# Performance work log

Hardware: AMD Instinct MI355X
Metric: run time of the kernel (lower is better)

The kernel has to match this reference:

```python
import jax, jax.numpy as jnp
import numpy as np
import math

B, L, D = 2, 2048, 512
D_INNER, D_STATE, D_CONV = 2 * D, 16, 4
DT_RANK = math.ceil(D / 16)  # 32


def setup_inputs() -> dict:
    key = jax.random.key(0)
    ks = jax.random.split(key, 9)
    s = 0.02
    x = jax.random.normal(ks[0], (B, L, D), dtype=jnp.float32)
    W_in = jax.random.normal(ks[1], (D, 2 * D_INNER), dtype=jnp.float32) * s
    conv_w = jax.random.normal(ks[2], (D_INNER, D_CONV), dtype=jnp.float32) * s
    conv_b = jnp.zeros((D_INNER,), dtype=jnp.float32)
    W_x = jax.random.normal(ks[3], (D_INNER, DT_RANK + 2 * D_STATE), dtype=jnp.float32) * s
    W_dt = jax.random.normal(ks[4], (DT_RANK, D_INNER), dtype=jnp.float32) * s
    b_dt = jax.random.normal(ks[5], (D_INNER,), dtype=jnp.float32) * s
    # S4D-real init: A = -[1..d_state] per channel
    A_log = jnp.log(jnp.broadcast_to(jnp.arange(1, D_STATE + 1, dtype=jnp.float32), (D_INNER, D_STATE)))
    D_param = jnp.ones((D_INNER,), dtype=jnp.float32)
    W_out = jax.random.normal(ks[6], (D_INNER, D), dtype=jnp.float32) * s
    return {"x": x, "W_in": W_in, "conv_w": conv_w, "conv_b": conv_b,
            "W_x": W_x, "W_dt": W_dt, "b_dt": b_dt, "A_log": A_log,
            "D_param": D_param, "W_out": W_out}


def _mamba(x, W_in, conv_w, conv_b, W_x, W_dt, b_dt, A_log, D_param, W_out):
    # in_proj -> [u, z]
    xz = jnp.einsum('bld,de->ble', x, W_in)
    u, z = jnp.split(xz, 2, axis=-1)  # each (B, L, d_inner)
    # depthwise causal conv1d along L
    u_c = jnp.transpose(u, (0, 2, 1))  # (B, d_inner, L)
    kern = conv_w[:, None, :]          # (d_inner, 1, d_conv)
    u_c = jax.lax.conv_general_dilated(
        u_c, kern, window_strides=(1,), padding=[(D_CONV - 1, 0)],
        feature_group_count=D_INNER,
        dimension_numbers=('NCH', 'OIH', 'NCH')) + conv_b[None, :, None]
    u = jax.nn.silu(jnp.transpose(u_c, (0, 2, 1)))  # (B, L, d_inner)
    # input-dependent dt, B, C
    x_dbl = jnp.einsum('bld,de->ble', u, W_x)
    dt_r = x_dbl[..., :DT_RANK]
    Bm = x_dbl[..., DT_RANK:DT_RANK + D_STATE]          # (B, L, d_state)
    Cm = x_dbl[..., DT_RANK + D_STATE:]                  # (B, L, d_state)
    dt = jax.nn.softplus(jnp.einsum('blr,rd->bld', dt_r, W_dt) + b_dt)  # (B, L, d_inner)
    A = -jnp.exp(A_log)  # (d_inner, d_state)

    def step(h, inp):
        dt_t, B_t, C_t, u_t = inp  # (B,d_inner), (B,d_state), (B,d_state), (B,d_inner)
        dA = jnp.exp(dt_t[:, :, None] * A)                      # (B, d_inner, d_state)
        h = h * dA + (dt_t * u_t)[:, :, None] * B_t[:, None, :]
        y = jnp.einsum('bds,bs->bd', h, C_t)
        return h, y

    h0 = jnp.zeros((B, D_INNER, D_STATE), dtype=x.dtype)
    xs = (jnp.transpose(dt, (1, 0, 2)), jnp.transpose(Bm, (1, 0, 2)),
          jnp.transpose(Cm, (1, 0, 2)), jnp.transpose(u, (1, 0, 2)))
    _, ys = jax.lax.scan(step, h0, xs)
    y = jnp.transpose(ys, (1, 0, 2)) + u * D_param  # (B, L, d_inner)
    y = y * jax.nn.silu(z)
    return jnp.einsum('bld,de->ble', y, W_out)


def reference(x, W_in, conv_w, conv_b, W_x, W_dt, b_dt, A_log, D_param, W_out):
    # MambaLayer.forward (eval): out = x + drop_path(mamba(x)); drop_path == Identity at eval
    return x + _mamba(x, W_in, conv_w, conv_b, W_x, W_dt, b_dt, A_log, D_param, W_out)
```

## Files before the change

kernel.cpp:

```cpp
#include <hip/hip_runtime.h>
#include <math.h>

#define BB 2
#define LL 2048
#define DD 512
#define DIN 1024
#define DXZ 2048
#define DSTATE 16
#define DTRANK 32
#define NDBL 64
#define ML (BB*LL)
#define LC2 64
#define NCH2 (LL/LC2)
#define CP 68

typedef __bf16 bf16_t;
typedef bf16_t bf16x8 __attribute__((ext_vector_type(8)));
typedef bf16_t bf16x4 __attribute__((ext_vector_type(4)));
typedef float f32x4 __attribute__((ext_vector_type(4)));

#define GBK 32
#define GBKP 40

__device__ __forceinline__ float fast_silu(float x) {
  return x * __builtin_amdgcn_rcpf(1.f + __builtin_amdgcn_exp2f(-1.44269504f * x));
}

template <int TM, int TN, int MODE, int CT>
__launch_bounds__(256)
__global__ void gemm_mfma(const bf16_t* __restrict__ A,
                          const bf16_t* __restrict__ Bt,
                          float* __restrict__ C, int ldc,
                          int M, int N, int K,
                          const float* __restrict__ aux) {
  __shared__ __align__(16) bf16_t As[TM * GBKP];
  __shared__ __align__(16) bf16_t Bs[TN * GBKP];
  const int tid = threadIdx.x;
  const int wid = tid >> 6, lane = tid & 63;
  const int q = lane >> 4, ln = lane & 15;
  constexpr int WM = TM / 2, WN = TN / 2;
  constexpr int FM = WM / 16, FN = WN / 16;
  const int wm = (wid >> 1) * WM, wn = (wid & 1) * WN;
  const int mBase = blockIdx.y * TM, nBase = blockIdx.x * TN;

  f32x4 acc[FM][FN] = {};

  for (int k0 = 0; k0 < K; k0 += GBK) {
#pragma unroll
    for (int i = 0; i < TM * GBK / (256 * 8); i++) {
      const int slot = tid + i * 256;
      const int m = slot >> 2, k8 = (slot & 3) * 8;
      *(bf16x8*)&As[m * GBKP + k8] =
          *(const bf16x8*)&A[(size_t)(mBase + m) * K + k0 + k8];
    }
#pragma unroll
    for (int i = 0; i < TN * GBK / (256 * 8); i++) {
      const int slot = tid + i * 256;
      const int n = slot >> 2, k8 = (slot & 3) * 8;
      *(bf16x8*)&Bs[n * GBKP + k8] =
          *(const bf16x8*)&Bt[(size_t)(nBase + n) * K + k0 + k8];
    }
    __syncthreads();
    bf16x8 af[FM], bfr[FN];
#pragma unroll
    for (int i = 0; i < FM; i++)
      af[i] = *(const bf16x8*)&As[(wm + i * 16 + ln) * GBKP + q * 8];
#pragma unroll
    for (int j = 0; j < FN; j++)
      bfr[j] = *(const bf16x8*)&Bs[(wn + j * 16 + ln) * GBKP + q * 8];
#pragma unroll
    for (int i = 0; i < FM; i++)
#pragma unroll
      for (int j = 0; j < FN; j++)
        acc[i][j] = __builtin_amdgcn_mfma_f32_16x16x32_bf16(
            af[i], bfr[j], acc[i][j], 0, 0, 0);
    __syncthreads();
  }

#pragma unroll
  for (int i = 0; i < FM; i++) {
    const int m0 = mBase + wm + i * 16 + q * 4;
#pragma unroll
    for (int j = 0; j < FN; j++) {
      const int n = nBase + wn + j * 16 + ln;
      if (CT == 1) {
        *(f32x4*)&C[(size_t)n * ldc + m0] = acc[i][j];
      } else {
#pragma unroll
        for (int r = 0; r < 4; r++) {
          float v = acc[i][j][r];
          if (MODE == 2) v += aux[(size_t)(m0 + r) * ldc + n];
          C[(size_t)(m0 + r) * ldc + n] = v;
        }
      }
    }
  }
}

__global__ void cast_bf16(const float* __restrict__ in, bf16_t* __restrict__ out,
                          int n4) {
  const int i = blockIdx.x * 256 + threadIdx.x;
  if (i >= n4) return;
  const float4 v = ((const float4*)in)[i];
  bf16x4 o = {(bf16_t)v.x, (bf16_t)v.y, (bf16_t)v.z, (bf16_t)v.w};
  ((bf16x4*)out)[i] = o;
}

__launch_bounds__(256)
__global__ void transpose_cast(const float* __restrict__ in, bf16_t* __restrict__ out,
                               int R, int C) {
  __shared__ float T[64][65];
  const int t = threadIdx.x;
  const int rB = blockIdx.y * 64, cB = blockIdx.x * 64;
  {
    const int r = t >> 4, c4 = (t & 15) * 4;
#pragma unroll
    for (int i = 0; i < 4; i++) {
      const float4 v = *(const float4*)&in[(size_t)(rB + r + i * 16) * C + cB + c4];
      T[r + i * 16][c4] = v.x;
      T[r + i * 16][c4 + 1] = v.y;
      T[r + i * 16][c4 + 2] = v.z;
      T[r + i * 16][c4 + 3] = v.w;
    }
  }
  __syncthreads();
  {
    const int c = t >> 2;
#pragma unroll
    for (int i = 0; i < 4; i++) {
      const int r0 = (t & 3) * 16 + i * 4;
      bf16x4 o = {(bf16_t)T[r0][c], (bf16_t)T[r0 + 1][c],
                  (bf16_t)T[r0 + 2][c], (bf16_t)T[r0 + 3][c]};
      *(bf16x4*)&out[(size_t)(cB + c) * R + rB + r0] = o;
    }
  }
}

template <int MODE, int AT, int CT>
__launch_bounds__(256)
__global__ void gemm_tiled(const float* __restrict__ A, int lda,
                           const float* __restrict__ B, int ldb,
                           float* __restrict__ C, int ldc,
                           int M, int N, int K,
                           const float* __restrict__ aux) {
  __shared__ float As[16][68];
  __shared__ float Bs[16][68];

  const int tid = threadIdx.x;
  const int tx = tid & 15, ty = tid >> 4;
  const int mBase = blockIdx.y * 64;
  const int nBase = blockIdx.x * 64;

  float acc[4][4] = {};

  for (int k0 = 0; k0 < K; k0 += 16) {
#pragma unroll
    for (int i = 0; i < 4; i++) {
      int idx = tid + i * 256;
      if (AT == 0) {
        int m = idx >> 4, kk = idx & 15;
        As[kk][m] = A[(size_t)(mBase + m) * lda + k0 + kk];
      } else {
        int kk = idx >> 6, m = idx & 63;
        As[kk][m] = A[(size_t)(k0 + kk) * lda + mBase + m];
      }
    }
#pragma unroll
    for (int i = 0; i < 4; i++) {
      int idx = tid + i * 256;
      int kk = idx >> 6, n = idx & 63;
      Bs[kk][n] = B[(size_t)(k0 + kk) * ldb + nBase + n];
    }
    __syncthreads();
#pragma unroll
    for (int kk = 0; kk < 16; kk++) {
      const float4 a4 = *reinterpret_cast<const float4*>(&As[kk][ty * 4]);
      const float4 b4 = *reinterpret_cast<const float4*>(&Bs[kk][tx * 4]);
      const float a[4] = {a4.x, a4.y, a4.z, a4.w};
      const float b[4] = {b4.x, b4.y, b4.z, b4.w};
#pragma unroll
      for (int i = 0; i < 4; i++)
#pragma unroll
        for (int j = 0; j < 4; j++) acc[i][j] = fmaf(a[i], b[j], acc[i][j]);
    }
    __syncthreads();
  }

  if (CT == 0) {
#pragma unroll
    for (int i = 0; i < 4; i++) {
      const int m = mBase + ty * 4 + i;
      const int n0 = nBase + tx * 4;
      float v[4];
#pragma unroll
      for (int j = 0; j < 4; j++) {
        float x = acc[i][j];
        if (MODE == 1) {
          x += aux[n0 + j];
          x = (x > 20.f) ? x
              : 0.69314718f * __builtin_amdgcn_logf(
                    1.f + __builtin_amdgcn_exp2f(x * 1.44269504f));
        }
        v[j] = x;
      }
      *reinterpret_cast<float4*>(&C[(size_t)m * ldc + n0]) =
          make_float4(v[0], v[1], v[2], v[3]);
    }
  } else {
    const int m0 = mBase + ty * 4;
#pragma unroll
    for (int j = 0; j < 4; j++) {
      const int n = nBase + tx * 4 + j;
      float v[4];
#pragma unroll
      for (int i = 0; i < 4; i++) {
        float x = acc[i][j];
        if (MODE == 1) {
          x += aux[n];
          x = (x > 20.f) ? x
              : 0.69314718f * __builtin_amdgcn_logf(
                    1.f + __builtin_amdgcn_exp2f(x * 1.44269504f));
        }
        v[i] = x;
      }
      *reinterpret_cast<float4*>(&C[(size_t)n * ldc + m0]) =
          make_float4(v[0], v[1], v[2], v[3]);
    }
  }
}

__launch_bounds__(256)
__global__ void conv_silu_T(const float* __restrict__ xzT,
                            const float* __restrict__ conv_w,
                            const float* __restrict__ conv_b,
                            float* __restrict__ uT) {
  const int idx = blockIdx.x * 256 + threadIdx.x;
  const int d = idx >> 10;
  const int ml0 = (idx & 1023) * 4;
  const int l0 = ml0 & (LL - 1);
  const float* row = xzT + (size_t)d * ML + ml0;
  const float4 Bv = *reinterpret_cast<const float4*>(row);
  float4 Av = make_float4(0.f, 0.f, 0.f, 0.f);
  if (l0 != 0) Av = *reinterpret_cast<const float4*>(row - 4);
  const float w0 = conv_w[d * 4 + 0], w1 = conv_w[d * 4 + 1];
  const float w2 = conv_w[d * 4 + 2], w3 = conv_w[d * 4 + 3];
  const float bias = conv_b[d];
  float o[4];
  o[0] = bias + w0 * Av.y + w1 * Av.z + w2 * Av.w + w3 * Bv.x;
  o[1] = bias + w0 * Av.z + w1 * Av.w + w2 * Bv.x + w3 * Bv.y;
  o[2] = bias + w0 * Av.w + w1 * Bv.x + w2 * Bv.y + w3 * Bv.z;
  o[3] = bias + w0 * Bv.x + w1 * Bv.y + w2 * Bv.z + w3 * Bv.w;
#pragma unroll
  for (int i = 0; i < 4; i++) o[i] = fast_silu(o[i]);
  *reinterpret_cast<float4*>(uT + (size_t)d * ML + ml0) =
      make_float4(o[0], o[1], o[2], o[3]);
}

__launch_bounds__(128, 3)
__global__ void scan_fused3(const float* __restrict__ dtT,
                            const float* __restrict__ uT,
                            float* __restrict__ xzT,
                            const float* __restrict__ xdbl,
                            const float* __restrict__ A_log,
                            const float* __restrict__ D_param) {
  __shared__ float dt_s[NCH2 * CP];
  __shared__ float u_s[NCH2 * CP];
  __shared__ float Pc[NCH2][DSTATE];
  __shared__ float Hc[NCH2][DSTATE];

  const int tid = threadIdx.x;
  const int c = blockIdx.x;
  const int b = c >> 10, d = c & (DIN - 1);
  const size_t rowoff = (size_t)d * ML + (size_t)b * LL;
  const float* dtrow = dtT + rowoff;
  const float* urow  = uT + rowoff;
  const float* zrow  = xzT + (size_t)(DIN + d) * ML + (size_t)b * LL;
  float* yrow = xzT + rowoff;

#pragma unroll
  for (int i = 0; i < 4; i++) {
    const int idx = (tid + i * 128) * 4;
    const int la = (idx >> 6) * CP + (idx & 63);
    *(float4*)&dt_s[la] = *(const float4*)&dtrow[idx];
    *(float4*)&u_s[la]  = *(const float4*)&urow[idx];
  }

  const int ch = tid >> 2, q = tid & 3;
  const int s0 = q * 4;
  float Al2[4];
#pragma unroll
  for (int k = 0; k < 4; k++)
    Al2[k] = -expf(A_log[d * DSTATE + s0 + k]) * 1.44269504f;
  const float* dp = dt_s + ch * CP;
  float* up = u_s + ch * CP;
  const float* BC = xdbl + ((size_t)b * LL + (size_t)ch * LC2) * NDBL + DTRANK + s0;
  __syncthreads();

  {
    float h0 = 0.f, h1 = 0.f, h2 = 0.f, h3 = 0.f, sdt = 0.f;
    float4 Bcur[4];
#pragma unroll
    for (int i = 0; i < 4; i++)
      Bcur[i] = *(const float4*)(BC + (size_t)i * NDBL);
    for (int g = 0; g < 16; g++) {
      float4 Bnxt[4];
#pragma unroll
      for (int i = 0; i < 4; i++)
        Bnxt[i] = *(const float4*)(BC + (size_t)((g + 1) * 4 + i) * NDBL);
#pragma unroll
      for (int i = 0; i < 4; i++) {
        const int l = g * 4 + i;
        const float dtv = dp[l];
        const float dtu = dtv * up[l];
        sdt += dtv;
        const float e0 = __builtin_amdgcn_exp2f(dtv * Al2[0]);
        const float e1 = __builtin_amdgcn_exp2f(dtv * Al2[1]);
        const float e2 = __builtin_amdgcn_exp2f(dtv * Al2[2]);
        const float e3 = __builtin_amdgcn_exp2f(dtv * Al2[3]);
        h0 = fmaf(h0, e0, dtu * Bcur[i].x);
        h1 = fmaf(h1, e1, dtu * Bcur[i].y);
        h2 = fmaf(h2, e2, dtu * Bcur[i].z);
        h3 = fmaf(h3, e3, dtu * Bcur[i].w);
      }
#pragma unroll
      for (int i = 0; i < 4; i++) Bcur[i] = Bnxt[i];
    }
    *(float4*)&Pc[ch][s0] = make_float4(
        __builtin_amdgcn_exp2f(Al2[0] * sdt), __builtin_amdgcn_exp2f(Al2[1] * sdt),
        __builtin_amdgcn_exp2f(Al2[2] * sdt), __builtin_amdgcn_exp2f(Al2[3] * sdt));
    *(float4*)&Hc[ch][s0] = make_float4(h0, h1, h2, h3);
  }
  __syncthreads();

  if (tid < DSTATE) {
    float h = 0.f;
#pragma unroll
    for (int k = 0; k < NCH2; k++) {
      const float Pv = Pc[k][tid], Hv = Hc[k][tid];
      Pc[k][tid] = h;
      h = fmaf(h, Pv, Hv);
    }
  }
  __syncthreads();

  {
    const float Dp = D_param[d];
    const float4 H4 = *(const float4*)&Pc[ch][s0];
    float h0 = H4.x, h1 = H4.y, h2 = H4.z, h3 = H4.w;
    float4 Bcur[4], Ccur[4];
#pragma unroll
    for (int i = 0; i < 4; i++) {
      Bcur[i] = *(const float4*)(BC + (size_t)i * NDBL);
      Ccur[i] = *(const float4*)(BC + (size_t)i * NDBL + DSTATE);
    }
    for (int g = 0; g < 16; g++) {
      float4 Bnxt[4], Cnxt[4];
#pragma unroll
      for (int i = 0; i < 4; i++) {
        Bnxt[i] = *(const float4*)(BC + (size_t)((g + 1) * 4 + i) * NDBL);
        Cnxt[i] = *(const float4*)(BC + (size_t)((g + 1) * 4 + i) * NDBL + DSTATE);
      }
#pragma unroll
      for (int i = 0; i < 4; i++) {
        const int l = g * 4 + i;
        const float dtv = dp[l];
        const float uv = up[l];
        const float dtu = dtv * uv;
        const float e0 = __builtin_amdgcn_exp2f(dtv * Al2[0]);
        const float e1 = __builtin_amdgcn_exp2f(dtv * Al2[1]);
        const float e2 = __builtin_amdgcn_exp2f(dtv * Al2[2]);
        const float e3 = __builtin_amdgcn_exp2f(dtv * Al2[3]);
        h0 = fmaf(h0, e0, dtu * Bcur[i].x);
        h1 = fmaf(h1, e1, dtu * Bcur[i].y);
        h2 = fmaf(h2, e2, dtu * Bcur[i].z);
        h3 = fmaf(h3, e3, dtu * Bcur[i].w);
        float p = fmaf(h0, Ccur[i].x,
                  fmaf(h1, Ccur[i].y, fmaf(h2, Ccur[i].z, h3 * Ccur[i].w)));
        p += __int_as_float(__builtin_amdgcn_ds_swizzle(__float_as_int(p), 0x041F));
        p += __int_as_float(__builtin_amdgcn_ds_swizzle(__float_as_int(p), 0x081F));
        if (q == (l & 3)) up[l] = p + uv * Dp;
      }
#pragma unroll
      for (int i = 0; i < 4; i++) { Bcur[i] = Bnxt[i]; Ccur[i] = Cnxt[i]; }
    }
  }
  __syncthreads();

#pragma unroll
  for (int i = 0; i < 4; i++) {
    const int idx = (tid + i * 128) * 4;
    const int la = (idx >> 6) * CP + (idx & 63);
    const float4 y4 = *(const float4*)&u_s[la];
    const float4 z4 = *(const float4*)&zrow[idx];
    float4 o;
    o.x = y4.x * fast_silu(z4.x);
    o.y = y4.y * fast_silu(z4.y);
    o.z = y4.z * fast_silu(z4.z);
    o.w = y4.w * fast_silu(z4.w);
    *(float4*)&yrow[idx] = o;
  }
}

extern "C" void kernel_launch(void* const* d_in, const int* in_sizes, int n_in,
                              void* d_out, int out_size, void* d_ws, size_t ws_size,
                              hipStream_t stream) {
  const float* x      = (const float*)d_in[0];
  const float* W_in   = (const float*)d_in[1];
  const float* conv_w = (const float*)d_in[2];
  const float* conv_b = (const float*)d_in[3];
  const float* W_x    = (const float*)d_in[4];
  const float* W_dt   = (const float*)d_in[5];
  const float* b_dt   = (const float*)d_in[6];
  const float* A_log  = (const float*)d_in[7];
  const float* D_par  = (const float*)d_in[8];
  const float* W_out  = (const float*)d_in[9];
  float* out = (float*)d_out;

  char* ws = (char*)d_ws;
  float* xzT   = (float*)(ws);
  float* uT    = (float*)(ws + (size_t)ML * DXZ * 4);
  float* x_dbl = (float*)(ws + (size_t)ML * (DXZ + DIN) * 4);
  char* dtT_b  = ws + (size_t)ML * (DXZ + DIN + NDBL) * 4;
  float* dtT   = (float*)dtT_b;
  bf16_t* u_b  = (bf16_t*)dtT_b;
  bf16_t* y_b  = (bf16_t*)(dtT_b + (size_t)ML * DIN * 2);
  char* extra  = ws + (size_t)ML * (DXZ + DIN + NDBL + DIN) * 4;
  bf16_t* x_b      = (bf16_t*)(extra);
  bf16_t* W_inT_b  = (bf16_t*)(extra + (size_t)ML * DD * 2);
  bf16_t* W_outT_b = (bf16_t*)(extra + (size_t)ML * DD * 2 + (size_t)DXZ * DD * 2);
  bf16_t* W_xT_b   = (bf16_t*)(extra + (size_t)ML * DD * 2 + (size_t)DXZ * DD * 2
                               + (size_t)DD * DIN * 2);

  cast_bf16<<<(ML * DD / 4) / 256, 256, 0, stream>>>(x, x_b, ML * DD / 4);
  transpose_cast<<<dim3(DXZ / 64, DD / 64), 256, 0, stream>>>(W_in, W_inT_b, DD, DXZ);
  transpose_cast<<<dim3(1, DIN / 64), 256, 0, stream>>>(W_x, W_xT_b, DIN, NDBL);
  transpose_cast<<<dim3(DD / 64, DIN / 64), 256, 0, stream>>>(W_out, W_outT_b, DIN, DD);

  gemm_mfma<128, 128, 0, 1><<<dim3(DXZ / 128, ML / 128), 256, 0, stream>>>(
      x_b, W_inT_b, xzT, ML, ML, DXZ, DD, nullptr);

  conv_silu_T<<<(DIN * (ML / 4)) / 256, 256, 0, stream>>>(xzT, conv_w, conv_b, uT);

  transpose_cast<<<dim3(ML / 64, DIN / 64), 256, 0, stream>>>(uT, u_b, DIN, ML);

  gemm_mfma<64, 64, 0, 0><<<dim3(1, ML / 64), 256, 0, stream>>>(
      u_b, W_xT_b, x_dbl, NDBL, ML, NDBL, DIN, nullptr);

  gemm_tiled<1, 0, 1><<<dim3(DIN / 64, ML / 64), 256, 0, stream>>>(
      x_dbl, NDBL, W_dt, DIN, dtT, ML, ML, DIN, DTRANK, b_dt);

  scan_fused3<<<BB * DIN, 128, 0, stream>>>(dtT, uT, xzT, x_dbl, A_log, D_par);

  transpose_cast<<<dim3(ML / 64, DIN / 64), 256, 0, stream>>>(xzT, y_b, DIN, ML);

  gemm_mfma<128, 64, 2, 0><<<dim3(DD / 64, ML / 128), 256, 0, stream>>>(
      y_b, W_outT_b, out, DD, ML, DD, DIN, x);
}
```

Before: 225.6 us.

## Fuse chunked scan into single pass with correction term, store xz and y in bf16

The scan drops its separate first pass over each chunk. It now runs one local scan per chunk starting from zero state, records the cumulative dt, then combines chunk states and adds a per-position correction C·(h_prev·exp(A·cumdt)). The in_proj output and the gated y are written in bf16, which halves traffic for the conv, the scan z read and the final transpose. Two channels share each 256-thread block. This removes one full sequential recurrence pass, in exchange for 16 extra exp2 per position and lower precision on the intermediate activations.

```diff
diff --git a/kernel.cpp b/kernel.cpp
--- a/kernel.cpp
+++ b/kernel.cpp
@@ -26,15 +26,17 @@
   return x * __builtin_amdgcn_rcpf(1.f + __builtin_amdgcn_exp2f(-1.44269504f * x));
 }
 
-template <int TM, int TN, int MODE, int CT>
+template <int TM, int TN, int MODE, int CT, int OB>
 __launch_bounds__(256)
 __global__ void gemm_mfma(const bf16_t* __restrict__ A,
                           const bf16_t* __restrict__ Bt,
-                          float* __restrict__ C, int ldc,
+                          void* __restrict__ Cv, int ldc,
                           int M, int N, int K,
                           const float* __restrict__ aux) {
   __shared__ __align__(16) bf16_t As[TM * GBKP];
   __shared__ __align__(16) bf16_t Bs[TN * GBKP];
+  float* C = (float*)Cv;
+  bf16_t* Cb = (bf16_t*)Cv;
   const int tid = threadIdx.x;
   const int wid = tid >> 6, lane = tid & 63;
   const int q = lane >> 4, ln = lane & 15;
@@ -84,7 +86,13 @@
     for (int j = 0; j < FN; j++) {
       const int n = nBase + wn + j * 16 + ln;
       if (CT == 1) {
-        *(f32x4*)&C[(size_t)n * ldc + m0] = acc[i][j];
+        if (OB == 1) {
+          bf16x4 o = {(bf16_t)acc[i][j][0], (bf16_t)acc[i][j][1],
+                      (bf16_t)acc[i][j][2], (bf16_t)acc[i][j][3]};
+          *(bf16x4*)&Cb[(size_t)n * ldc + m0] = o;
+        } else {
+          *(f32x4*)&C[(size_t)n * ldc + m0] = acc[i][j];
+        }
       } else {
 #pragma unroll
         for (int r = 0; r < 4; r++) {
@@ -106,8 +114,9 @@
   ((bf16x4*)out)[i] = o;
 }
 
+template <typename TIN>
 __launch_bounds__(256)
-__global__ void transpose_cast(const float* __restrict__ in, bf16_t* __restrict__ out,
+__global__ void transpose_cast(const TIN* __restrict__ in, bf16_t* __restrict__ out,
                                int R, int C) {
   __shared__ float T[64][65];
   const int t = threadIdx.x;
@@ -116,11 +125,19 @@
     const int r = t >> 4, c4 = (t & 15) * 4;
 #pragma unroll
     for (int i = 0; i < 4; i++) {
-      const float4 v = *(const float4*)&in[(size_t)(rB + r + i * 16) * C + cB + c4];
-      T[r + i * 16][c4] = v.x;
-      T[r + i * 16][c4 + 1] = v.y;
-      T[r + i * 16][c4 + 2] = v.z;
-      T[r + i * 16][c4 + 3] = v.w;
+      const TIN* src = &in[(size_t)(rB + r + i * 16) * C + cB + c4];
+      float v0, v1, v2, v3;
+      if (sizeof(TIN) == 4) {
+        const float4 v = *(const float4*)src;
+        v0 = v.x; v1 = v.y; v2 = v.z; v3 = v.w;
+      } else {
+        const bf16x4 v = *(const bf16x4*)src;
+        v0 = (float)v[0]; v1 = (float)v[1]; v2 = (float)v[2]; v3 = (float)v[3];
+      }
+      T[r + i * 16][c4] = v0;
+      T[r + i * 16][c4 + 1] = v1;
+      T[r + i * 16][c4 + 2] = v2;
+      T[r + i * 16][c4 + 3] = v3;
     }
   }
   __syncthreads();
@@ -230,7 +247,7 @@
 }
 
 __launch_bounds__(256)
-__global__ void conv_silu_T(const float* __restrict__ xzT,
+__global__ void conv_silu_T(const bf16_t* __restrict__ xzTb,
                             const float* __restrict__ conv_w,
                             const float* __restrict__ conv_b,
                             float* __restrict__ uT) {
@@ -238,115 +255,79 @@
   const int d = idx >> 10;
   const int ml0 = (idx & 1023) * 4;
   const int l0 = ml0 & (LL - 1);
-  const float* row = xzT + (size_t)d * ML + ml0;
-  const float4 Bv = *reinterpret_cast<const float4*>(row);
-  float4 Av = make_float4(0.f, 0.f, 0.f, 0.f);
-  if (l0 != 0) Av = *reinterpret_cast<const float4*>(row - 4);
+  const bf16_t* row = xzTb + (size_t)d * ML + ml0;
+  const bf16x4 Bv4 = *(const bf16x4*)row;
+  bf16x4 Av4 = {(bf16_t)0.f, (bf16_t)0.f, (bf16_t)0.f, (bf16_t)0.f};
+  if (l0 != 0) Av4 = *(const bf16x4*)(row - 4);
+  const float Ay = (float)Av4[1], Az = (float)Av4[2], Aw = (float)Av4[3];
+  const float Bx = (float)Bv4[0], By = (float)Bv4[1], Bz = (float)Bv4[2],
+              Bw = (float)Bv4[3];
   const float w0 = conv_w[d * 4 + 0], w1 = conv_w[d * 4 + 1];
   const float w2 = conv_w[d * 4 + 2], w3 = conv_w[d * 4 + 3];
   const float bias = conv_b[d];
   float o[4];
-  o[0] = bias + w0 * Av.y + w1 * Av.z + w2 * Av.w + w3 * Bv.x;
-  o[1] = bias + w0 * Av.z + w1 * Av.w + w2 * Bv.x + w3 * Bv.y;
-  o[2] = bias + w0 * Av.w + w1 * Bv.x + w2 * Bv.y + w3 * Bv.z;
-  o[3] = bias + w0 * Bv.x + w1 * Bv.y + w2 * Bv.z + w3 * Bv.w;
+  o[0] = bias + w0 * Ay + w1 * Az + w2 * Aw + w3 * Bx;
+  o[1] = bias + w0 * Az + w1 * Aw + w2 * Bx + w3 * By;
+  o[2] = bias + w0 * Aw + w1 * Bx + w2 * By + w3 * Bz;
+  o[3] = bias + w0 * Bx + w1 * By + w2 * Bz + w3 * Bw;
 #pragma unroll
   for (int i = 0; i < 4; i++) o[i] = fast_silu(o[i]);
   *reinterpret_cast<float4*>(uT + (size_t)d * ML + ml0) =
       make_float4(o[0], o[1], o[2], o[3]);
 }
 
-__launch_bounds__(128, 3)
-__global__ void scan_fused3(const float* __restrict__ dtT,
+__launch_bounds__(256, 3)
+__global__ void scan_fused4(const float* __restrict__ dtT,
                             const float* __restrict__ uT,
-                            float* __restrict__ xzT,
+                            const bf16_t* __restrict__ xzTb,
+                            bf16_t* __restrict__ yTb,
                             const float* __restrict__ xdbl,
                             const float* __restrict__ A_log,
                             const float* __restrict__ D_param) {
-  __shared__ float dt_s[NCH2 * CP];
-  __shared__ float u_s[NCH2 * CP];
-  __shared__ float Pc[NCH2][DSTATE];
-  __shared__ float Hc[NCH2][DSTATE];
+  __shared__ float dt_s[2][NCH2 * CP];
+  __shared__ float u_s[2][NCH2 * CP];
+  __shared__ float Pc[2][NCH2][DSTATE];
+  __shared__ float Hc[2][NCH2][DSTATE];
+  __shared__ float Al2s[2][DSTATE];
 
   const int tid = threadIdx.x;
-  const int c = blockIdx.x;
+  const int half = tid >> 7;
+  const int ht = tid & 127;
+  const int c = blockIdx.x * 2 + half;
   const int b = c >> 10, d = c & (DIN - 1);
   const size_t rowoff = (size_t)d * ML + (size_t)b * LL;
   const float* dtrow = dtT + rowoff;
   const float* urow  = uT + rowoff;
-  const float* zrow  = xzT + (size_t)(DIN + d) * ML + (size_t)b * LL;
-  float* yrow = xzT + rowoff;
+  const bf16_t* zrow = xzTb + (size_t)(DIN + d) * ML + (size_t)b * LL;
+  bf16_t* yrow = yTb + rowoff;
+
+  float* dts = dt_s[half];
+  float* us  = u_s[half];
 
 #pragma unroll
   for (int i = 0; i < 4; i++) {
-    const int idx = (tid + i * 128) * 4;
+    const int idx = (ht + i * 128) * 4;
     const int la = (idx >> 6) * CP + (idx & 63);
-    *(float4*)&dt_s[la] = *(const float4*)&dtrow[idx];
-    *(float4*)&u_s[la]  = *(const float4*)&urow[idx];
-  }
-
-  const int ch = tid >> 2, q = tid & 3;
+    *(float4*)&dts[la] = *(const float4*)&dtrow[idx];
+    *(float4*)&us[la]  = *(const float4*)&urow[idx];
+  }
+  if (ht < DSTATE)
+    Al2s[half][ht] = -expf(A_log[d * DSTATE + ht]) * 1.44269504f;
+
+  const int ch = ht >> 2, q = ht & 3;
   const int s0 = q * 4;
+  const float* BC = xdbl + ((size_t)b * LL + (size_t)ch * LC2) * NDBL + DTRANK + s0;
+  const float Dp = D_param[d];
+  __syncthreads();
+
   float Al2[4];
 #pragma unroll
-  for (int k = 0; k < 4; k++)
-    Al2[k] = -expf(A_log[d * DSTATE + s0 + k]) * 1.44269504f;
-  const float* dp = dt_s + ch * CP;
-  float* up = u_s + ch * CP;
-  const float* BC = xdbl + ((size_t)b * LL + (size_t)ch * LC2) * NDBL + DTRANK + s0;
-  __syncthreads();
+  for (int k = 0; k < 4; k++) Al2[k] = Al2s[half][s0 + k];
 
   {
+    float* dp = dts + ch * CP;
+    float* up = us + ch * CP;
     float h0 = 0.f, h1 = 0.f, h2 = 0.f, h3 = 0.f, sdt = 0.f;
-    float4 Bcur[4];
-#pragma unroll
-    for (int i = 0; i < 4; i++)
-      Bcur[i] = *(const float4*)(BC + (size_t)i * NDBL);
-    for (int g = 0; g < 16; g++) {
-      float4 Bnxt[4];
-#pragma unroll
-      for (int i = 0; i < 4; i++)
-        Bnxt[i] = *(const float4*)(BC + (size_t)((g + 1) * 4 + i) * NDBL);
-#pragma unroll
-      for (int i = 0; i < 4; i++) {
-        const int l = g * 4 + i;
-        const float dtv = dp[l];
-        const float dtu = dtv * up[l];
-        sdt += dtv;
-        const float e0 = __builtin_amdgcn_exp2f(dtv * Al2[0]);
-        const float e1 = __builtin_amdgcn_exp2f(dtv * Al2[1]);
-        const float e2 = __builtin_amdgcn_exp2f(dtv * Al2[2]);
-        const float e3 = __builtin_amdgcn_exp2f(dtv * Al2[3]);
-        h0 = fmaf(h0, e0, dtu * Bcur[i].x);
-        h1 = fmaf(h1, e1, dtu * Bcur[i].y);
-        h2 = fmaf(h2, e2, dtu * Bcur[i].z);
-        h3 = fmaf(h3, e3, dtu * Bcur[i].w);
-      }
-#pragma unroll
-      for (int i = 0; i < 4; i++) Bcur[i] = Bnxt[i];
-    }
-    *(float4*)&Pc[ch][s0] = make_float4(
-        __builtin_amdgcn_exp2f(Al2[0] * sdt), __builtin_amdgcn_exp2f(Al2[1] * sdt),
-        __builtin_amdgcn_exp2f(Al2[2] * sdt), __builtin_amdgcn_exp2f(Al2[3] * sdt));
-    *(float4*)&Hc[ch][s0] = make_float4(h0, h1, h2, h3);
-  }
-  __syncthreads();
-
-  if (tid < DSTATE) {
-    float h = 0.f;
-#pragma unroll
-    for (int k = 0; k < NCH2; k++) {
-      const float Pv = Pc[k][tid], Hv = Hc[k][tid];
-      Pc[k][tid] = h;
-      h = fmaf(h, Pv, Hv);
-    }
-  }
-  __syncthreads();
-
-  {
-    const float Dp = D_param[d];
-    const float4 H4 = *(const float4*)&Pc[ch][s0];
-    float h0 = H4.x, h1 = H4.y, h2 = H4.z, h3 = H4.w;
     float4 Bcur[4], Ccur[4];
 #pragma unroll
     for (int i = 0; i < 4; i++) {
@@ -354,11 +335,12 @@
       Ccur[i] = *(const float4*)(BC + (size_t)i * NDBL + DSTATE);
     }
     for (int g = 0; g < 16; g++) {
-      float4 Bnxt[4], Cnxt[4];
+      const int gn = (g < 15) ? g + 1 : 15;
+      float4 Bn[4], Cn[4];
 #pragma unroll
       for (int i = 0; i < 4; i++) {
-        Bnxt[i] = *(const float4*)(BC + (size_t)((g + 1) * 4 + i) * NDBL);
-        Cnxt[i] = *(const float4*)(BC + (size_t)((g + 1) * 4 + i) * NDBL + DSTATE);
+        Bn[i] = *(const float4*)(BC + (size_t)(gn * 4 + i) * NDBL);
+        Cn[i] = *(const float4*)(BC + (size_t)(gn * 4 + i) * NDBL + DSTATE);
       }
 #pragma unroll
       for (int i = 0; i < 4; i++) {
@@ -366,6 +348,7 @@
         const float dtv = dp[l];
         const float uv = up[l];
         const float dtu = dtv * uv;
+        sdt += dtv;
         const float e0 = __builtin_amdgcn_exp2f(dtv * Al2[0]);
         const float e1 = __builtin_amdgcn_exp2f(dtv * Al2[1]);
         const float e2 = __builtin_amdgcn_exp2f(dtv * Al2[2]);
@@ -378,26 +361,84 @@
                   fmaf(h1, Ccur[i].y, fmaf(h2, Ccur[i].z, h3 * Ccur[i].w)));
         p += __int_as_float(__builtin_amdgcn_ds_swizzle(__float_as_int(p), 0x041F));
         p += __int_as_float(__builtin_amdgcn_ds_swizzle(__float_as_int(p), 0x081F));
-        if (q == (l & 3)) up[l] = p + uv * Dp;
-      }
-#pragma unroll
-      for (int i = 0; i < 4; i++) { Bcur[i] = Bnxt[i]; Ccur[i] = Cnxt[i]; }
-    }
+        if (q == i) {
+          up[l] = p + uv * Dp;
+          dp[l] = sdt;
+        }
+      }
+#pragma unroll
+      for (int i = 0; i < 4; i++) { Bcur[i] = Bn[i]; Ccur[i] = Cn[i]; }
+    }
+    *(float4*)&Pc[half][ch][s0] = make_float4(
+        __builtin_amdgcn_exp2f(Al2[0] * sdt), __builtin_amdgcn_exp2f(Al2[1] * sdt),
+        __builtin_amdgcn_exp2f(Al2[2] * sdt), __builtin_amdgcn_exp2f(Al2[3] * sdt));
+    *(float4*)&Hc[half][ch][s0] = make_float4(h0, h1, h2, h3);
   }
   __syncthreads();
 
+  if (ht < DSTATE) {
+    float h = 0.f;
+#pragma unroll
+    for (int k = 0; k < NCH2; k++) {
+      const float Pv = Pc[half][k][ht], Hv = Hc[half][k][ht];
+      Pc[half][k][ht] = h;
+      h = fmaf(h, Pv, Hv);
+    }
+  }
+  __syncthreads();
+
+  {
+    float A16[16];
+#pragma unroll
+    for (int s = 0; s < 16; s++) A16[s] = Al2s[half][s];
+#pragma unroll 4
+    for (int i = 0; i < 16; i++) {
+      const int l = ht + i * 128;
+      const int ck = l >> 6;
+      const int la = ck * CP + (l & 63);
+      const float sdt = dts[la];
+      const float* Crow = xdbl + ((size_t)b * LL + l) * NDBL + DTRANK + DSTATE;
+      const float4 C0 = *(const float4*)(Crow + 0);
+      const float4 C1 = *(const float4*)(Crow + 4);
+      const float4 C2 = *(const float4*)(Crow + 8);
+      const float4 C3 = *(const float4*)(Crow + 12);
+      const float4 g0 = *(const float4*)&Pc[half][ck][0];
+      const float4 g1 = *(const float4*)&Pc[half][ck][4];
+      const float4 g2 = *(const float4*)&Pc[half][ck][8];
+      const float4 g3 = *(const float4*)&Pc[half][ck][12];
+      float corr = 0.f;
+      corr = fmaf(C0.x * g0.x, __builtin_amdgcn_exp2f(A16[0] * sdt), corr);
+      corr = fmaf(C0.y * g0.y, __builtin_amdgcn_exp2f(A16[1] * sdt), corr);
+      corr = fmaf(C0.z * g0.z, __builtin_amdgcn_exp2f(A16[2] * sdt), corr);
+      corr = fmaf(C0.w * g0.w, __builtin_amdgcn_exp2f(A16[3] * sdt), corr);
+      corr = fmaf(C1.x * g1.x, __builtin_amdgcn_exp2f(A16[4] * sdt), corr);
+      corr = fmaf(C1.y * g1.y, __builtin_amdgcn_exp2f(A16[5] * sdt), corr);
+      corr = fmaf(C1.z * g1.z, __builtin_amdgcn_exp2f(A16[6] * sdt), corr);
+      corr = fmaf(C1.w * g1.w, __builtin_amdgcn_exp2f(A16[7] * sdt), corr);
+      corr = fmaf(C2.x * g2.x, __builtin_amdgcn_exp2f(A16[8] * sdt), corr);
+      corr = fmaf(C2.y * g2.y, __builtin_amdgcn_exp2f(A16[9] * sdt), corr);
+      corr = fmaf(C2.z * g2.z, __builtin_amdgcn_exp2f(A16[10] * sdt), corr);
+      corr = fmaf(C2.w * g2.w, __builtin_amdgcn_exp2f(A16[11] * sdt), corr);
+      corr = fmaf(C3.x * g3.x, __builtin_amdgcn_exp2f(A16[12] * sdt), corr);
+      corr = fmaf(C3.y * g3.y, __builtin_amdgcn_exp2f(A16[13] * sdt), corr);
+      corr = fmaf(C3.z * g3.z, __builtin_amdgcn_exp2f(A16[14] * sdt), corr);
+      corr = fmaf(C3.w * g3.w, __builtin_amdgcn_exp2f(A16[15] * sdt), corr);
+      us[la] += corr;
+    }
+  }
+  __syncthreads();
+
 #pragma unroll
   for (int i = 0; i < 4; i++) {
-    const int idx = (tid + i * 128) * 4;
+    const int idx = (ht + i * 128) * 4;
     const int la = (idx >> 6) * CP + (idx & 63);
-    const float4 y4 = *(const float4*)&u_s[la];
-    const float4 z4 = *(const float4*)&zrow[idx];
-    float4 o;
-    o.x = y4.x * fast_silu(z4.x);
-    o.y = y4.y * fast_silu(z4.y);
-    o.z = y4.z * fast_silu(z4.z);
-    o.w = y4.w * fast_silu(z4.w);
-    *(float4*)&yrow[idx] = o;
+    const float4 y4 = *(const float4*)&us[la];
+    const bf16x4 z4 = *(const bf16x4*)&zrow[idx];
+    bf16x4 o = {(bf16_t)(y4.x * fast_silu((float)z4[0])),
+                (bf16_t)(y4.y * fast_silu((float)z4[1])),
+                (bf16_t)(y4.z * fast_silu((float)z4[2])),
+                (bf16_t)(y4.w * fast_silu((float)z4[3]))};
+    *(bf16x4*)&yrow[idx] = o;
   }
 }
 
@@ -416,43 +457,42 @@
   const float* W_out  = (const float*)d_in[9];
   float* out = (float*)d_out;
 
+  const size_t MB = 1 << 20;
   char* ws = (char*)d_ws;
-  float* xzT   = (float*)(ws);
-  float* uT    = (float*)(ws + (size_t)ML * DXZ * 4);
-  float* x_dbl = (float*)(ws + (size_t)ML * (DXZ + DIN) * 4);
-  char* dtT_b  = ws + (size_t)ML * (DXZ + DIN + NDBL) * 4;
-  float* dtT   = (float*)dtT_b;
-  bf16_t* u_b  = (bf16_t*)dtT_b;
-  bf16_t* y_b  = (bf16_t*)(dtT_b + (size_t)ML * DIN * 2);
-  char* extra  = ws + (size_t)ML * (DXZ + DIN + NDBL + DIN) * 4;
-  bf16_t* x_b      = (bf16_t*)(extra);
-  bf16_t* W_inT_b  = (bf16_t*)(extra + (size_t)ML * DD * 2);
-  bf16_t* W_outT_b = (bf16_t*)(extra + (size_t)ML * DD * 2 + (size_t)DXZ * DD * 2);
-  bf16_t* W_xT_b   = (bf16_t*)(extra + (size_t)ML * DD * 2 + (size_t)DXZ * DD * 2
-                               + (size_t)DD * DIN * 2);
+  bf16_t* xzTb = (bf16_t*)ws;
+  float* uT    = (float*)(ws + 16 * MB);
+  float* x_dbl = (float*)(ws + 32 * MB);
+  float* dtT   = (float*)(ws + 33 * MB);
+  bf16_t* u_b  = (bf16_t*)(ws + 49 * MB);
+  bf16_t* y_b  = (bf16_t*)(ws + 49 * MB);
+  bf16_t* yTb  = (bf16_t*)(ws + 57 * MB);
+  bf16_t* x_b      = (bf16_t*)(ws + 65 * MB);
+  bf16_t* W_inT_b  = (bf16_t*)(ws + 69 * MB);
+  bf16_t* W_outT_b = (bf16_t*)(ws + 71 * MB);
+  bf16_t* W_xT_b   = (bf16_t*)(ws + 72 * MB);
 
   cast_bf16<<<(ML * DD / 4) / 256, 256, 0, stream>>>(x, x_b, ML * DD / 4);
-  transpose_cast<<<dim3(DXZ / 64, DD / 64), 256, 0, stream>>>(W_in, W_inT_b, DD, DXZ);
-  transpose_cast<<<dim3(1, DIN / 64), 256, 0, stream>>>(W_x, W_xT_b, DIN, NDBL);
-  transpose_cast<<<dim3(DD / 64, DIN / 64), 256, 0, stream>>>(W_out, W_outT_b, DIN, DD);
-
-  gemm_mfma<128, 128, 0, 1><<<dim3(DXZ / 128, ML / 128), 256, 0, stream>>>(
-      x_b, W_inT_b, xzT, ML, ML, DXZ, DD, nullptr);
-
-  conv_silu_T<<<(DIN * (ML / 4)) / 256, 256, 0, stream>>>(xzT, conv_w, conv_b, uT);
-
-  transpose_cast<<<dim3(ML / 64, DIN / 64), 256, 0, stream>>>(uT, u_b, DIN, ML);
-
-  gemm_mfma<64, 64, 0, 0><<<dim3(1, ML / 64), 256, 0, stream>>>(
+  transpose_cast<float><<<dim3(DXZ / 64, DD / 64), 256, 0, stream>>>(W_in, W_inT_b, DD, DXZ);
+  transpose_cast<float><<<dim3(1, DIN / 64), 256, 0, stream>>>(W_x, W_xT_b, DIN, NDBL);
+  transpose_cast<float><<<dim3(DD / 64, DIN / 64), 256, 0, stream>>>(W_out, W_outT_b, DIN, DD);
+
+  gemm_mfma<128, 128, 0, 1, 1><<<dim3(DXZ / 128, ML / 128), 256, 0, stream>>>(
+      x_b, W_inT_b, xzTb, ML, ML, DXZ, DD, nullptr);
+
+  conv_silu_T<<<(DIN * (ML / 4)) / 256, 256, 0, stream>>>(xzTb, conv_w, conv_b, uT);
+
+  transpose_cast<float><<<dim3(ML / 64, DIN / 64), 256, 0, stream>>>(uT, u_b, DIN, ML);
+
+  gemm_mfma<64, 64, 0, 0, 0><<<dim3(1, ML / 64), 256, 0, stream>>>(
       u_b, W_xT_b, x_dbl, NDBL, ML, NDBL, DIN, nullptr);
 
   gemm_tiled<1, 0, 1><<<dim3(DIN / 64, ML / 64), 256, 0, stream>>>(
       x_dbl, NDBL, W_dt, DIN, dtT, ML, ML, DIN, DTRANK, b_dt);
 
-  scan_fused3<<<BB * DIN, 128, 0, stream>>>(dtT, uT, xzT, x_dbl, A_log, D_par);
-
-  transpose_cast<<<dim3(ML / 64, DIN / 64), 256, 0, stream>>>(xzT, y_b, DIN, ML);
-
-  gemm_mfma<128, 64, 2, 0><<<dim3(DD / 64, ML / 128), 256, 0, stream>>>(
+  scan_fused4<<<BB * DIN / 2, 256, 0, stream>>>(dtT, uT, xzTb, yTb, x_dbl, A_log, D_par);
+
+  transpose_cast<bf16_t><<<dim3(ML / 64, DIN / 64), 256, 0, stream>>>(yTb, y_b, DIN, ML);
+
+  gemm_mfma<128, 64, 2, 0, 0><<<dim3(DD / 64, ML / 128), 256, 0, stream>>>(
       y_b, W_outT_b, out, DD, ML, DD, DIN, x);
 }
```

Measured after the change: 234.6 us. 1.04x slower.
